# Optimization experiments

Hardware: AMD Instinct MI355X
Metric: run time of the kernel (lower is better)

## Reference

```python
import jax, jax.numpy as jnp
from jax import lax
import numpy as np


def setup_inputs() -> dict:
    key = jax.random.key(0)
    k1, k2 = jax.random.split(key)
    sat_features = jax.random.normal(k1, (128, 4, 64, 16), dtype=jnp.float32)  # [B_s, h, w, c]
    grd_features = jax.random.normal(k2, (128, 4, 64, 16), dtype=jnp.float32)  # [B_g, h, gw, c]
    return {"sat_features": sat_features, "grd_features": grd_features}


def reference(sat_features, grd_features):
    B_s, h, w, c = sat_features.shape
    B_g, gh, gw, gc = grd_features.shape
    assert h == gh and c == gc

    # --- corr: circular cross-correlation over width via conv2d ---
    n = gw - 1
    sat_pad = jnp.concatenate([sat_features, sat_features[:, :, :n, :]], axis=2)  # [B_s,h,w+n,c]
    rhs = jnp.transpose(grd_features, (1, 2, 3, 0))  # HWIO: [h,gw,c,B_g]
    out = lax.conv_general_dilated(
        sat_pad, rhs, window_strides=(1, 1), padding='VALID',
        dimension_numbers=('NHWC', 'HWIO', 'NHWC'))  # [B_s,1,w,B_g]
    corr = out[:, 0, :, :]                  # [B_s, w, B_g]
    orien = jnp.argmax(corr, axis=1)        # [B_s, B_g] int

    # --- crop_sat: circular-shift gather along width, crop to grd width ---
    shift = orien % w                                                   # [B_s,B_g]
    idx = (jnp.arange(gw)[None, None, :] + shift[:, :, None]) % w       # [B_s,B_g,gw]
    # gather: sat_crop[i,j,y,k,ch] = sat_features[i, y, idx[i,j,k], ch]
    sat_crop = jnp.take_along_axis(
        sat_features[:, None],              # [B_s,1,h,w,c]
        idx[:, :, None, :, None],           # [B_s,B_g,1,gw,1]
        axis=3)                             # -> [B_s,B_g,h,gw,c]

    # --- L2 normalize per (sat,grd) pair and squared-chord distance ---
    norm = jnp.sqrt(jnp.sum(sat_crop * sat_crop, axis=(2, 3, 4), keepdims=True))
    sat_matrix = sat_crop / jnp.maximum(norm, 1e-12)
    dot = jnp.sum(sat_matrix * grd_features[None], axis=(2, 3, 4))      # [B_s,B_g]
    distance = 2.0 - 2.0 * dot.T                                        # [B_g,B_s]

    return sat_features, grd_features, distance, orien
```

## Files before the change

kernel.cpp:

```cpp
#include <hip/hip_runtime.h>
#include <math.h>

typedef _Float16 f16;
typedef __attribute__((ext_vector_type(8))) _Float16 f16x8;
typedef __attribute__((ext_vector_type(16))) float f32x16;

#define DIST_OFF  1048576
#define ORI_OFF   1064960
#define SATP_STR  72

#define MFMA(a,b,c) __builtin_amdgcn_mfma_f32_32x32x16_f16((a),(b),(c),0,0,0)

__global__ __launch_bounds__(256) void prep_k(const float* __restrict__ grd,
                                              f16* __restrict__ gHi, f16* __restrict__ gLo,
                                              const float4* __restrict__ satIn,
                                              const float4* __restrict__ grdIn,
                                              float4* __restrict__ out4) {
    const int b = blockIdx.x;
    if (b >= 64) {
        int i = (b - 64) * 256 + threadIdx.x;
        out4[i] = satIn[i];
        out4[131072 + i] = grdIn[i];
        return;
    }
    __shared__ f16 tH[8192], tL[8192];
    const int tid = threadIdx.x;
    const int g0 = (b & 7) * 16;
    const int kq = b >> 3;
    #pragma unroll
    for (int i = 0; i < 32; ++i) {
        int flat = i * 256 + tid;
        int g_l = flat >> 9;
        int r   = flat & 511;
        int h   = r >> 7;
        int j   = r & 127;
        float v = grd[(((g0 + g_l) * 4 + h) * 64 + kq * 8) * 16 + j];
        int k_l = (j >> 4) * 64 + h * 16 + (j & 15);
        f16 hv = (f16)v;
        int a = (k_l >> 3) * 128 + g_l * 8 + (k_l & 7);
        tH[a] = hv;
        tL[a] = (f16)(v - (float)hv);
    }
    __syncthreads();
    #pragma unroll
    for (int i = 0; i < 4; ++i) {
        int f = i * 256 + tid;
        int dst = (kq * 64 + (f >> 4)) * 128 + g0 + (f & 15);
        ((f16x8*)gHi)[dst] = *(const f16x8*)(tH + f * 8);
        ((f16x8*)gLo)[dst] = *(const f16x8*)(tL + f * 8);
    }
}

__global__ __launch_bounds__(512, 2) void corr_k(const float* __restrict__ sat,
                                                 const f16* __restrict__ gHi,
                                                 const f16* __restrict__ gLo,
                                                 float* __restrict__ out) {
    __shared__ __align__(16) unsigned char smem[131072];
    __shared__ float wred[8];
    __shared__ float rnormS;
    f16* sH = (f16*)smem;
    f16* sL = sH + 127 * SATP_STR;
    float* red = (float*)smem;

    const int tid = threadIdx.x;
    const int s  = blockIdx.x >> 1;
    const int gh = blockIdx.x & 1;
    const int wave = tid >> 6, lane = tid & 63;
    const int m = lane & 31, half = lane >> 5;

    const float* satS = sat + s * 4096;
    float ssq = 0.f;
    #pragma unroll
    for (int r = 0; r < 8; ++r) {
        int idx = r * 512 + tid;
        float v = satS[idx];
        int h = idx >> 10, w = (idx >> 4) & 63, c = idx & 15;
        int col = h * 16 + c;
        f16 hv = (f16)v, lv = (f16)(v - (float)hv);
        sH[w * SATP_STR + col] = hv;
        sL[w * SATP_STR + col] = lv;
        if (w < 63) { sH[(w + 64) * SATP_STR + col] = hv; sL[(w + 64) * SATP_STR + col] = lv; }
        ssq += v * v;
    }
    #pragma unroll
    for (int off = 32; off > 0; off >>= 1) ssq += __shfl_down(ssq, off, 64);
    if (lane == 0) wred[wave] = ssq;
    __syncthreads();
    if (tid == 0) {
        float t = 0.f;
        #pragma unroll
        for (int i = 0; i < 8; ++i) t += wred[i];
        rnormS = 1.f / fmaxf(sqrtf(t), 1e-12f);
    }

    const f16* A0h = sH + m * SATP_STR + half * 8;
    const f16* A0l = sL + m * SATP_STR + half * 8;
    const f16x8* BHp = (const f16x8*)gHi;
    const f16x8* BLp = (const f16x8*)gLo;
    const int ggBase = half * 128 + gh * 64 + m;

    f32x16 z;
    #pragma unroll
    for (int r = 0; r < 16; ++r) z[r] = 0.f;
    f32x16 h00 = z, h01 = z, h10 = z, h11 = z, x00 = z, x01 = z, x10 = z, x11 = z;

    f16x8 ah[2][2], al[2][2], bh[2][2], bl[2][2];

#define LOADT(p, t) { \
    int tc = (t) > 255 ? 255 : (t); \
    int ao = (tc >> 2) * SATP_STR + (tc & 3) * 16; \
    ah[p][0] = *(const f16x8*)(A0h + ao); \
    ah[p][1] = *(const f16x8*)(A0h + ao + 32 * SATP_STR); \
    al[p][0] = *(const f16x8*)(A0l + ao); \
    al[p][1] = *(const f16x8*)(A0l + ao + 32 * SATP_STR); \
    int bu = tc * 256 + ggBase; \
    bh[p][0] = BHp[bu]; bh[p][1] = BHp[bu + 32]; \
    bl[p][0] = BLp[bu]; bl[p][1] = BLp[bu + 32]; }

#define STEP(p) { \
    h00 = MFMA(ah[p][0], bh[p][0], h00); \
    h01 = MFMA(ah[p][0], bh[p][1], h01); \
    h10 = MFMA(ah[p][1], bh[p][0], h10); \
    h11 = MFMA(ah[p][1], bh[p][1], h11); \
    x00 = MFMA(ah[p][0], bl[p][0], x00); x00 = MFMA(al[p][0], bh[p][0], x00); \
    x01 = MFMA(ah[p][0], bl[p][1], x01); x01 = MFMA(al[p][0], bh[p][1], x01); \
    x10 = MFMA(ah[p][1], bl[p][0], x10); x10 = MFMA(al[p][1], bh[p][0], x10); \
    x11 = MFMA(ah[p][1], bl[p][1], x11); x11 = MFMA(al[p][1], bh[p][1], x11); }

    const int t0 = wave * 32;
    LOADT(0, t0)
    #pragma unroll 4
    for (int t = t0; t < t0 + 32; t += 2) {
        LOADT(1, t + 1)
        STEP(0)
        LOADT(0, t + 2)
        STEP(1)
    }
    h00 = h00 + x00; h01 = h01 + x01; h10 = h10 + x10; h11 = h11 + x11;

    __syncthreads();
    float* rw = red + wave * 4096;
    #pragma unroll
    for (int r = 0; r < 16; ++r) {
        int j0 = (r & 3) + 8 * (r >> 2) + 4 * half;
        rw[j0 * 64 + m]             = h00[r];
        rw[j0 * 64 + 32 + m]        = h01[r];
        rw[(j0 + 32) * 64 + m]      = h10[r];
        rw[(j0 + 32) * 64 + 32 + m] = h11[r];
    }
    __syncthreads();
    #pragma unroll
    for (int i = 0; i < 8; ++i) {
        int c = i * 512 + tid;
        float v = red[c]         + red[c + 4096]  + red[c + 8192]  + red[c + 12288]
                + red[c + 16384] + red[c + 20480] + red[c + 24576] + red[c + 28672];
        red[c] = v;
    }
    __syncthreads();

    if (tid < 64) {
        int g = tid;
        float best = red[g];
        int bj = 0;
        for (int j = 1; j < 64; ++j) {
            float v = red[j * 64 + g];
            if (v > best) { best = v; bj = j; }
        }
        float dot = best * rnormS;
        int gg = gh * 64 + g;
        out[DIST_OFF + gg * 128 + s] = 2.f - 2.f * dot;
        out[ORI_OFF + s * 128 + gg]  = (float)bj;
    }
}

__global__ void copy_k(const float4* __restrict__ a, const float4* __restrict__ b,
                       float4* __restrict__ out) {
    int i = blockIdx.x * 256 + threadIdx.x;
    out[i] = a[i];
    out[131072 + i] = b[i];
}

extern "C" void kernel_launch(void* const* d_in, const int* in_sizes, int n_in,
                              void* d_out, int out_size, void* d_ws, size_t ws_size,
                              hipStream_t stream) {
    const float* sat = (const float*)d_in[0];
    const float* grd = (const float*)d_in[1];
    float* out = (float*)d_out;

    const bool useWs = (ws_size >= (size_t)2 * 1024 * 1024);
    f16* gHi;
    f16* gLo;
    if (useWs) {
        gHi = (f16*)d_ws;
        gLo = gHi + 524288;
    } else {
        gHi = (f16*)out;
        gLo = (f16*)(out + 262144);
    }

    prep_k<<<useWs ? 576 : 64, 256, 0, stream>>>(grd, gHi, gLo,
                                                 (const float4*)sat, (const float4*)grd,
                                                 (float4*)out);
    corr_k<<<256, 512, 0, stream>>>(sat, gHi, gLo, out);
    if (!useWs)
        copy_k<<<512, 256, 0, stream>>>((const float4*)sat, (const float4*)grd, (float4*)out);
}
```

Measured before the change: 86.89 us.

## Split corr kernel across 16 waves with tree reduction in smaller shared memory

The correlation kernel now runs 1024 threads per block, so each wave handles 16 K-steps instead of 32. The separate split-precision accumulators are merged into four, dropping the software double-buffered loads. The 8-way shared-memory sum is replaced by a staged pairwise tree reduction through padded, XOR-swizzled tiles, which cuts LDS use from 128KB to 68KB. The argmax is then done in registers with a cross-half shuffle. The launcher always stages the fp16 grd copies in the output buffer and copies the inputs in a separate third kernel, which adds a launch and a serial copy pass.

```diff
diff --git a/kernel.cpp b/kernel.cpp
--- a/kernel.cpp
+++ b/kernel.cpp
@@ -8,22 +8,15 @@
 #define DIST_OFF  1048576
 #define ORI_OFF   1064960
 #define SATP_STR  72
+#define RTS       68
 
 #define MFMA(a,b,c) __builtin_amdgcn_mfma_f32_32x32x16_f16((a),(b),(c),0,0,0)
+#define RIDX(g, j0) ((g) * RTS + ((j0) ^ ((((g) >> 3) & 1) << 4)))
 
 __global__ __launch_bounds__(256) void prep_k(const float* __restrict__ grd,
-                                              f16* __restrict__ gHi, f16* __restrict__ gLo,
-                                              const float4* __restrict__ satIn,
-                                              const float4* __restrict__ grdIn,
-                                              float4* __restrict__ out4) {
+                                              f16* __restrict__ gHi, f16* __restrict__ gLo) {
+    __shared__ f16 tH[8192], tL[8192];
     const int b = blockIdx.x;
-    if (b >= 64) {
-        int i = (b - 64) * 256 + threadIdx.x;
-        out4[i] = satIn[i];
-        out4[131072 + i] = grdIn[i];
-        return;
-    }
-    __shared__ f16 tH[8192], tL[8192];
     const int tid = threadIdx.x;
     const int g0 = (b & 7) * 16;
     const int kq = b >> 3;
@@ -51,12 +44,12 @@
     }
 }
 
-__global__ __launch_bounds__(512, 2) void corr_k(const float* __restrict__ sat,
-                                                 const f16* __restrict__ gHi,
-                                                 const f16* __restrict__ gLo,
-                                                 float* __restrict__ out) {
-    __shared__ __align__(16) unsigned char smem[131072];
-    __shared__ float wred[8];
+__global__ __launch_bounds__(1024, 4) void corr_k(const float* __restrict__ sat,
+                                                  const f16* __restrict__ gHi,
+                                                  const f16* __restrict__ gLo,
+                                                  float* __restrict__ out) {
+    __shared__ __align__(16) unsigned char smem[69632];
+    __shared__ float wred[16];
     __shared__ float rnormS;
     f16* sH = (f16*)smem;
     f16* sL = sH + 127 * SATP_STR;
@@ -71,8 +64,8 @@
     const float* satS = sat + s * 4096;
     float ssq = 0.f;
     #pragma unroll
-    for (int r = 0; r < 8; ++r) {
-        int idx = r * 512 + tid;
+    for (int r = 0; r < 4; ++r) {
+        int idx = r * 1024 + tid;
         float v = satS[idx];
         int h = idx >> 10, w = (idx >> 4) & 63, c = idx & 15;
         int col = h * 16 + c;
@@ -89,7 +82,7 @@
     if (tid == 0) {
         float t = 0.f;
         #pragma unroll
-        for (int i = 0; i < 8; ++i) t += wred[i];
+        for (int i = 0; i < 16; ++i) t += wred[i];
         rnormS = 1.f / fmaxf(sqrtf(t), 1e-12f);
     }
 
@@ -99,77 +92,104 @@
     const f16x8* BLp = (const f16x8*)gLo;
     const int ggBase = half * 128 + gh * 64 + m;
 
-    f32x16 z;
-    #pragma unroll
-    for (int r = 0; r < 16; ++r) z[r] = 0.f;
-    f32x16 h00 = z, h01 = z, h10 = z, h11 = z, x00 = z, x01 = z, x10 = z, x11 = z;
-
-    f16x8 ah[2][2], al[2][2], bh[2][2], bl[2][2];
-
-#define LOADT(p, t) { \
-    int tc = (t) > 255 ? 255 : (t); \
-    int ao = (tc >> 2) * SATP_STR + (tc & 3) * 16; \
-    ah[p][0] = *(const f16x8*)(A0h + ao); \
-    ah[p][1] = *(const f16x8*)(A0h + ao + 32 * SATP_STR); \
-    al[p][0] = *(const f16x8*)(A0l + ao); \
-    al[p][1] = *(const f16x8*)(A0l + ao + 32 * SATP_STR); \
-    int bu = tc * 256 + ggBase; \
-    bh[p][0] = BHp[bu]; bh[p][1] = BHp[bu + 32]; \
-    bl[p][0] = BLp[bu]; bl[p][1] = BLp[bu + 32]; }
-
-#define STEP(p) { \
-    h00 = MFMA(ah[p][0], bh[p][0], h00); \
-    h01 = MFMA(ah[p][0], bh[p][1], h01); \
-    h10 = MFMA(ah[p][1], bh[p][0], h10); \
-    h11 = MFMA(ah[p][1], bh[p][1], h11); \
-    x00 = MFMA(ah[p][0], bl[p][0], x00); x00 = MFMA(al[p][0], bh[p][0], x00); \
-    x01 = MFMA(ah[p][0], bl[p][1], x01); x01 = MFMA(al[p][0], bh[p][1], x01); \
-    x10 = MFMA(ah[p][1], bl[p][0], x10); x10 = MFMA(al[p][1], bh[p][0], x10); \
-    x11 = MFMA(ah[p][1], bl[p][1], x11); x11 = MFMA(al[p][1], bh[p][1], x11); }
-
-    const int t0 = wave * 32;
-    LOADT(0, t0)
+    f32x16 acc[2][2];
+    #pragma unroll
+    for (int jt = 0; jt < 2; ++jt)
+        #pragma unroll
+        for (int gt = 0; gt < 2; ++gt)
+            #pragma unroll
+            for (int r = 0; r < 16; ++r) acc[jt][gt][r] = 0.f;
+
+    const int t0 = wave * 16;
     #pragma unroll 4
-    for (int t = t0; t < t0 + 32; t += 2) {
-        LOADT(1, t + 1)
-        STEP(0)
-        LOADT(0, t + 2)
-        STEP(1)
-    }
-    h00 = h00 + x00; h01 = h01 + x01; h10 = h10 + x10; h11 = h11 + x11;
-
-    __syncthreads();
-    float* rw = red + wave * 4096;
-    #pragma unroll
-    for (int r = 0; r < 16; ++r) {
-        int j0 = (r & 3) + 8 * (r >> 2) + 4 * half;
-        rw[j0 * 64 + m]             = h00[r];
-        rw[j0 * 64 + 32 + m]        = h01[r];
-        rw[(j0 + 32) * 64 + m]      = h10[r];
-        rw[(j0 + 32) * 64 + 32 + m] = h11[r];
-    }
-    __syncthreads();
-    #pragma unroll
-    for (int i = 0; i < 8; ++i) {
-        int c = i * 512 + tid;
-        float v = red[c]         + red[c + 4096]  + red[c + 8192]  + red[c + 12288]
-                + red[c + 16384] + red[c + 20480] + red[c + 24576] + red[c + 28672];
-        red[c] = v;
-    }
-    __syncthreads();
-
-    if (tid < 64) {
-        int g = tid;
-        float best = red[g];
-        int bj = 0;
-        for (int j = 1; j < 64; ++j) {
-            float v = red[j * 64 + g];
-            if (v > best) { best = v; bj = j; }
+    for (int t = t0; t < t0 + 16; ++t) {
+        int ao = (t >> 2) * SATP_STR + (t & 3) * 16;
+        f16x8 ah0 = *(const f16x8*)(A0h + ao);
+        f16x8 ah1 = *(const f16x8*)(A0h + ao + 32 * SATP_STR);
+        f16x8 al0 = *(const f16x8*)(A0l + ao);
+        f16x8 al1 = *(const f16x8*)(A0l + ao + 32 * SATP_STR);
+        int bu = t * 256 + ggBase;
+        f16x8 bh0 = BHp[bu], bh1 = BHp[bu + 32];
+        f16x8 bl0 = BLp[bu], bl1 = BLp[bu + 32];
+        acc[0][0] = MFMA(ah0, bh0, acc[0][0]);
+        acc[0][1] = MFMA(ah0, bh1, acc[0][1]);
+        acc[1][0] = MFMA(ah1, bh0, acc[1][0]);
+        acc[1][1] = MFMA(ah1, bh1, acc[1][1]);
+        acc[0][0] = MFMA(ah0, bl0, acc[0][0]);
+        acc[0][1] = MFMA(ah0, bl1, acc[0][1]);
+        acc[1][0] = MFMA(ah1, bl0, acc[1][0]);
+        acc[1][1] = MFMA(ah1, bl1, acc[1][1]);
+        acc[0][0] = MFMA(al0, bh0, acc[0][0]);
+        acc[0][1] = MFMA(al0, bh1, acc[0][1]);
+        acc[1][0] = MFMA(al1, bh0, acc[1][0]);
+        acc[1][1] = MFMA(al1, bh1, acc[1][1]);
+    }
+
+#define WTILE(T) { float* tp = red + (T) * 4352; \
+    _Pragma("unroll") for (int jt = 0; jt < 2; ++jt) \
+    _Pragma("unroll") for (int gt = 0; gt < 2; ++gt) { \
+        int g = gt * 32 + m; \
+        _Pragma("unroll") for (int q = 0; q < 4; ++q) { \
+            int j0 = jt * 32 + 8 * q + 4 * half; \
+            float4 v = { acc[jt][gt][4*q], acc[jt][gt][4*q+1], acc[jt][gt][4*q+2], acc[jt][gt][4*q+3] }; \
+            *(float4*)(tp + RIDX(g, j0)) = v; } } }
+
+#define ATILE(T) { const float* tp = red + (T) * 4352; \
+    _Pragma("unroll") for (int jt = 0; jt < 2; ++jt) \
+    _Pragma("unroll") for (int gt = 0; gt < 2; ++gt) { \
+        int g = gt * 32 + m; \
+        _Pragma("unroll") for (int q = 0; q < 4; ++q) { \
+            int j0 = jt * 32 + 8 * q + 4 * half; \
+            float4 v = *(const float4*)(tp + RIDX(g, j0)); \
+            acc[jt][gt][4*q] += v.x; acc[jt][gt][4*q+1] += v.y; \
+            acc[jt][gt][4*q+2] += v.z; acc[jt][gt][4*q+3] += v.w; } } }
+
+    __syncthreads();
+    if (wave >= 8 && wave < 12) WTILE(wave - 8)
+    __syncthreads();
+    if (wave < 4) ATILE(wave)
+    __syncthreads();
+    if (wave >= 12) WTILE(wave - 12)
+    __syncthreads();
+    if (wave >= 4 && wave < 8) ATILE(wave - 4)
+    __syncthreads();
+    if (wave >= 4 && wave < 8) WTILE(wave - 4)
+    __syncthreads();
+    if (wave < 4) ATILE(wave)
+    __syncthreads();
+    if (wave == 2 || wave == 3) WTILE(wave - 2)
+    __syncthreads();
+    if (wave < 2) ATILE(wave)
+    __syncthreads();
+    if (wave == 1) WTILE(0)
+    __syncthreads();
+
+    if (wave == 0) {
+        ATILE(0)
+        #pragma unroll
+        for (int gt = 0; gt < 2; ++gt) {
+            float best = -1e30f;
+            int bj = 0;
+            #pragma unroll
+            for (int jt = 0; jt < 2; ++jt)
+                #pragma unroll
+                for (int q = 0; q < 4; ++q)
+                    #pragma unroll
+                    for (int i = 0; i < 4; ++i) {
+                        int j = jt * 32 + 8 * q + 4 * half + i;
+                        float v = acc[jt][gt][4 * q + i];
+                        if (v > best) { best = v; bj = j; }
+                    }
+            float ob = __shfl_xor(best, 32, 64);
+            int  obj = __shfl_xor(bj, 32, 64);
+            if (ob > best || (ob == best && obj < bj)) { best = ob; bj = obj; }
+            if ((half == 0) == (gt == 0)) {
+                int g = gh * 64 + gt * 32 + m;
+                float dot = best * rnormS;
+                out[DIST_OFF + g * 128 + s] = 2.f - 2.f * dot;
+                out[ORI_OFF + s * 128 + g]  = (float)bj;
+            }
         }
-        float dot = best * rnormS;
-        int gg = gh * 64 + g;
-        out[DIST_OFF + gg * 128 + s] = 2.f - 2.f * dot;
-        out[ORI_OFF + s * 128 + gg]  = (float)bj;
     }
 }
 
@@ -187,21 +207,10 @@
     const float* grd = (const float*)d_in[1];
     float* out = (float*)d_out;
 
-    const bool useWs = (ws_size >= (size_t)2 * 1024 * 1024);
-    f16* gHi;
-    f16* gLo;
-    if (useWs) {
-        gHi = (f16*)d_ws;
-        gLo = gHi + 524288;
-    } else {
-        gHi = (f16*)out;
-        gLo = (f16*)(out + 262144);
-    }
-
-    prep_k<<<useWs ? 576 : 64, 256, 0, stream>>>(grd, gHi, gLo,
-                                                 (const float4*)sat, (const float4*)grd,
-                                                 (float4*)out);
-    corr_k<<<256, 512, 0, stream>>>(sat, gHi, gLo, out);
-    if (!useWs)
-        copy_k<<<512, 256, 0, stream>>>((const float4*)sat, (const float4*)grd, (float4*)out);
-}
+    f16* gHi = (f16*)out;
+    f16* gLo = (f16*)(out + 262144);
+
+    prep_k<<<64, 256, 0, stream>>>(grd, gHi, gLo);
+    corr_k<<<256, 1024, 0, stream>>>(sat, gHi, gLo, out);
+    copy_k<<<512, 256, 0, stream>>>((const float4*)sat, (const float4*)grd, (float4*)out);
+}
```

Result: slower. 91.38 us (+5.2%).
